# Kernel optimization log

Measured on AMD Instinct MI355X. Metric: run time of the kernel, lower is better.

## Reference

```python
import jax, jax.numpy as jnp
import numpy as np

DIM = 1024
DEPTH = 6
HEADS = 16
MLP_DIM = 4096
EPS = 1e-5


def setup_inputs() -> dict:
    key = jax.random.key(0)
    ks = jax.random.split(key, 8)
    d, L, f = DIM, DEPTH, MLP_DIM
    s = lambda fan_in: 1.0 / np.sqrt(fan_in)
    inp = {
        "x": jax.random.normal(ks[0], (4, 1024, d), dtype=jnp.float32),
        "ln1_w": jnp.ones((L, d), jnp.float32),
        "ln1_b": jnp.zeros((L, d), jnp.float32),
        "qkv_w": jax.random.normal(ks[1], (L, d, 3 * d), jnp.float32) * s(d),
        "qkv_b": jnp.zeros((L, 3 * d), jnp.float32),
        "proj_w": jax.random.normal(ks[2], (L, d, d), jnp.float32) * s(d),
        "proj_b": jnp.zeros((L, d), jnp.float32),
        "ln2_w": jnp.ones((L, d), jnp.float32),
        "ln2_b": jnp.zeros((L, d), jnp.float32),
        "mlp_w1": jax.random.normal(ks[3], (L, d, f), jnp.float32) * s(d),
        "mlp_b1": jax.random.normal(ks[4], (L, f), jnp.float32) * 1e-6,
        "mlp_w2": jax.random.normal(ks[5], (L, f, d), jnp.float32) * s(f),
        "mlp_b2": jax.random.normal(ks[6], (L, d), jnp.float32) * 1e-6,
    }
    return inp


def _layer_norm(x, w, b):
    mu = jnp.mean(x, axis=-1, keepdims=True)
    var = jnp.mean(jnp.square(x - mu), axis=-1, keepdims=True)
    return (x - mu) * jax.lax.rsqrt(var + EPS) * w + b


def _block(x, ln1_w, ln1_b, qkv_w, qkv_b, proj_w, proj_b,
           ln2_w, ln2_b, mlp_w1, mlp_b1, mlp_w2, mlp_b2):
    b, n, d = x.shape
    h = HEADS
    hd = d // h
    scale = d ** (-0.5)  # note: original scales by dim**-0.5, not head_dim**-0.5
    # attention sublayer (pre-LN + residual)
    y = _layer_norm(x, ln1_w, ln1_b)
    qkv = y @ qkv_w + qkv_b                      # [b, n, 3d]
    qkv = qkv.reshape(b, n, 3, h, hd)            # matches 'b n (qkv h d)'
    q, k, v = (jnp.moveaxis(qkv[:, :, i], 1, 2) for i in range(3))  # [b, h, n, hd]
    dots = jnp.einsum('bhid,bhjd->bhij', q, k) * scale
    attn = jax.nn.softmax(dots, axis=-1)
    out = jnp.einsum('bhij,bhjd->bhid', attn, v)
    out = jnp.moveaxis(out, 1, 2).reshape(b, n, d)
    x = x + out @ proj_w + proj_b
    # MLP sublayer (pre-LN + residual)
    y = _layer_norm(x, ln2_w, ln2_b)
    y = jax.nn.gelu(y @ mlp_w1 + mlp_b1, approximate=False)
    x = x + y @ mlp_w2 + mlp_b2
    return x


def reference(x, ln1_w, ln1_b, qkv_w, qkv_b, proj_w, proj_b,
              ln2_w, ln2_b, mlp_w1, mlp_b1, mlp_w2, mlp_b2):
    for l in range(DEPTH):
        x = _block(x, ln1_w[l], ln1_b[l], qkv_w[l], qkv_b[l],
                   proj_w[l], proj_b[l], ln2_w[l], ln2_b[l],
                   mlp_w1[l], mlp_b1[l], mlp_w2[l], mlp_b2[l])
    return x
```

## Files before the change

### kernel.cpp

```cpp
#include <hip/hip_runtime.h>

typedef __attribute__((ext_vector_type(8))) short short8;
typedef __attribute__((ext_vector_type(4))) float floatx4;

#define DIM   1024
#define SEQ   1024
#define BATCH 4
#define NHEAD 16
#define HDIM  64
#define MLPD  4096
#define DEPTH 6
#define MTOK  (BATCH*SEQ)

__device__ __forceinline__ unsigned short f2bf(float f) {
    union { float f; unsigned u; } v; v.f = f;
    unsigned r = v.u + 0x7fffu + ((v.u >> 16) & 1u);
    return (unsigned short)(r >> 16);
}

__device__ __forceinline__ void gld16(const void* g, void* l) {
    __builtin_amdgcn_global_load_lds(
        (const __attribute__((address_space(1))) unsigned int*)g,
        (__attribute__((address_space(3))) unsigned int*)l, 16, 0, 0);
}

__global__ __launch_bounds__(256) void ln_kernel(
    const float* __restrict__ x, const float* __restrict__ w,
    const float* __restrict__ b, unsigned short* __restrict__ y)
{
    __shared__ float red[8];
    const int row = blockIdx.x;
    const int t = threadIdx.x;
    const float4 v = ((const float4*)(x + (size_t)row * DIM))[t];
    float s = v.x + v.y + v.z + v.w;
#pragma unroll
    for (int m = 1; m < 64; m <<= 1) s += __shfl_xor(s, m);
    if ((t & 63) == 0) red[t >> 6] = s;
    __syncthreads();
    const float mu = (red[0] + red[1] + red[2] + red[3]) * (1.0f / DIM);
    const float d0 = v.x - mu, d1 = v.y - mu, d2 = v.z - mu, d3 = v.w - mu;
    float q = d0 * d0 + d1 * d1 + d2 * d2 + d3 * d3;
#pragma unroll
    for (int m = 1; m < 64; m <<= 1) q += __shfl_xor(q, m);
    if ((t & 63) == 0) red[4 + (t >> 6)] = q;
    __syncthreads();
    const float var = (red[4] + red[5] + red[6] + red[7]) * (1.0f / DIM);
    const float rs = rsqrtf(var + 1e-5f);
    const float4 wv = ((const float4*)w)[t];
    const float4 bv = ((const float4*)b)[t];
    ushort4 o;
    o.x = f2bf(d0 * rs * wv.x + bv.x);
    o.y = f2bf(d1 * rs * wv.y + bv.y);
    o.z = f2bf(d2 * rs * wv.z + bv.z);
    o.w = f2bf(d3 * rs * wv.w + bv.w);
    ((ushort4*)(y + (size_t)row * DIM))[t] = o;
}

__global__ __launch_bounds__(256) void wtrans_kernel(
    const float* __restrict__ W, unsigned short* __restrict__ Wt, int K, int N)
{
    __shared__ float tile[64][65];
    const int n0 = blockIdx.x * 64, k0 = blockIdx.y * 64;
    const int t = threadIdx.x;
#pragma unroll
    for (int p = t; p < 1024; p += 256) {
        const int k = p >> 4, nq = (p & 15) * 4;
        const float4 v = *(const float4*)&W[(size_t)(k0 + k) * N + n0 + nq];
        tile[k][nq + 0] = v.x; tile[k][nq + 1] = v.y;
        tile[k][nq + 2] = v.z; tile[k][nq + 3] = v.w;
    }
    __syncthreads();
#pragma unroll
    for (int p = t; p < 1024; p += 256) {
        const int n = p >> 4, kq = (p & 15) * 4;
        ushort4 o;
        o.x = f2bf(tile[kq + 0][n]); o.y = f2bf(tile[kq + 1][n]);
        o.z = f2bf(tile[kq + 2][n]); o.w = f2bf(tile[kq + 3][n]);
        *(ushort4*)&Wt[(size_t)(n0 + n) * K + k0 + kq] = o;
    }
}

template <int MODE>
__global__ __launch_bounds__(256) void gemm_pipe(
    const unsigned short* __restrict__ A, const unsigned short* __restrict__ Bt,
    const float* __restrict__ bias, void* __restrict__ Cout,
    int M, int K, int N)
{
    __shared__ __align__(16) unsigned short Al[2 * 128 * 32];
    __shared__ __align__(16) unsigned short Bl[2 * 128 * 32];

    const int bm = blockIdx.y * 128, bn = blockIdx.x * 128;
    const int tid = threadIdx.x;
    const int lane = tid & 63, wid = tid >> 6;
    const int lm = lane & 15, quad = lane >> 4;
    const int wm = (wid >> 1) * 64, wn = (wid & 1) * 64;

    floatx4 acc[4][4] = {};

    const unsigned short* gA = A + (size_t)(bm + wid * 32 + (lane >> 2)) * K + (lane & 3) * 8;
    const unsigned short* gB = Bt + (size_t)(bn + wid * 32 + (lane >> 2)) * K + (lane & 3) * 8;
    const int wof = wid * 1024;

    gld16(gA, &Al[wof]);
    gld16(gA + (size_t)16 * K, &Al[wof + 512]);
    gld16(gB, &Bl[wof]);
    gld16(gB + (size_t)16 * K, &Bl[wof + 512]);

    const int nk = K >> 5;
    for (int i = 0; i < nk; i++) {
        __syncthreads();
        const int cur = (i & 1) * 4096;
        if (i + 1 < nk) {
            const int nxt = ((i + 1) & 1) * 4096;
            const int kt = (i + 1) * 32;
            gld16(gA + kt, &Al[nxt + wof]);
            gld16(gA + (size_t)16 * K + kt, &Al[nxt + wof + 512]);
            gld16(gB + kt, &Bl[nxt + wof]);
            gld16(gB + (size_t)16 * K + kt, &Bl[nxt + wof + 512]);
        }
        short8 af[4], bf[4];
#pragma unroll
        for (int t = 0; t < 4; t++)
            af[t] = *(const short8*)&Al[cur + (wm + t * 16 + lm) * 32 + quad * 8];
#pragma unroll
        for (int t = 0; t < 4; t++)
            bf[t] = *(const short8*)&Bl[cur + (wn + t * 16 + lm) * 32 + quad * 8];
#pragma unroll
        for (int t = 0; t < 4; t++)
#pragma unroll
            for (int j = 0; j < 4; j++)
                acc[t][j] = __builtin_amdgcn_mfma_f32_16x16x32_bf16(
                    af[t], bf[j], acc[t][j], 0, 0, 0);
    }

#pragma unroll
    for (int i = 0; i < 4; i++) {
        const int row = bm + wm + i * 16 + quad * 4;
#pragma unroll
        for (int j = 0; j < 4; j++) {
            const int col = bn + wn + j * 16 + lm;
            const float bb = bias[col];
#pragma unroll
            for (int r = 0; r < 4; r++) {
                float v = acc[i][j][r] + bb;
                const size_t idx = (size_t)(row + r) * N + col;
                if constexpr (MODE == 0) {
                    ((unsigned short*)Cout)[idx] = f2bf(v);
                } else if constexpr (MODE == 1) {
                    const float g = 0.5f * v * (1.0f + erff(v * 0.70710678118654752f));
                    ((unsigned short*)Cout)[idx] = f2bf(g);
                } else {
                    ((float*)Cout)[idx] += v;
                }
            }
        }
    }
}

__global__ __launch_bounds__(256) void vtrans_kernel(
    const unsigned short* __restrict__ qkv, unsigned short* __restrict__ Vt)
{
    __shared__ unsigned short tile[64][65];
    const int bh = blockIdx.x, nt = blockIdx.y;
    const int b = bh >> 4, h = bh & 15;
    const int t = threadIdx.x;
#pragma unroll
    for (int p = t; p < 4096; p += 256) {
        const int n = p >> 6, c = p & 63;
        tile[n][c] = qkv[(size_t)(b * SEQ + nt * 64 + n) * (3 * DIM) + 2 * DIM + h * HDIM + c];
    }
    __syncthreads();
#pragma unroll
    for (int p = t; p < 4096; p += 256) {
        const int hd = p >> 6, n = p & 63;
        Vt[((size_t)bh * HDIM + hd) * SEQ + nt * 64 + n] = tile[n][hd];
    }
}

__global__ __launch_bounds__(256) void attn_kernel(
    const unsigned short* __restrict__ qkv, const unsigned short* __restrict__ Vt,
    unsigned short* __restrict__ O)
{
    __shared__ __align__(16) unsigned short P[2][4][16 * 40];
    const int bh = blockIdx.x;
    const int b = bh >> 4, h = bh & 15;
    const int tid = threadIdx.x, lane = tid & 63, wid = tid >> 6;
    const int lm = lane & 15, quad = lane >> 4;
    const int q0 = (blockIdx.y * 4 + wid) * 16;

    const unsigned short* Qbase = qkv + (size_t)(b * SEQ) * (3 * DIM) + h * HDIM;
    const unsigned short* Kbase = Qbase + DIM;
    const unsigned short* Vbase = Vt + (size_t)bh * HDIM * SEQ;

    short8 aq[2];
#pragma unroll
    for (int t = 0; t < 2; t++)
        aq[t] = *(const short8*)&Qbase[(size_t)(q0 + lm) * (3 * DIM) + t * 32 + quad * 8];

    short8 ones;
#pragma unroll
    for (int t = 0; t < 8; t++) ones[t] = (short)0x3F80;

    floatx4 o[4] = {};
    floatx4 sacc = {};
    const float scale = 0.03125f;
    const float M = 3.0f;

    short8 k0f[4], v0f[4], k1f[4], v1f[4];

    auto loadKV = [&](short8* kf, short8* vf, int kt) {
#pragma unroll
        for (int s = 0; s < 2; s++)
#pragma unroll
            for (int t = 0; t < 2; t++)
                kf[s * 2 + t] = *(const short8*)&Kbase[(size_t)(kt + s * 16 + lm) * (3 * DIM) + t * 32 + quad * 8];
#pragma unroll
        for (int ti = 0; ti < 4; ti++)
            vf[ti] = *(const short8*)&Vbase[(size_t)(ti * 16 + lm) * SEQ + kt + quad * 8];
    };

    auto compute = [&](const short8* kf, const short8* vf, unsigned short* Pw) {
        floatx4 s0 = {}, s1 = {};
        s0 = __builtin_amdgcn_mfma_f32_16x16x32_bf16(aq[0], kf[0], s0, 0, 0, 0);
        s0 = __builtin_amdgcn_mfma_f32_16x16x32_bf16(aq[1], kf[1], s0, 0, 0, 0);
        s1 = __builtin_amdgcn_mfma_f32_16x16x32_bf16(aq[0], kf[2], s1, 0, 0, 0);
        s1 = __builtin_amdgcn_mfma_f32_16x16x32_bf16(aq[1], kf[3], s1, 0, 0, 0);
#pragma unroll
        for (int r = 0; r < 4; r++) {
            Pw[(quad * 4 + r) * 40 + lm]      = f2bf(__expf(fmaf(s0[r], scale, -M)));
            Pw[(quad * 4 + r) * 40 + 16 + lm] = f2bf(__expf(fmaf(s1[r], scale, -M)));
        }
        const short8 pa = *(const short8*)&Pw[lm * 40 + quad * 8];
        sacc = __builtin_amdgcn_mfma_f32_16x16x32_bf16(pa, ones, sacc, 0, 0, 0);
#pragma unroll
        for (int ti = 0; ti < 4; ti++)
            o[ti] = __builtin_amdgcn_mfma_f32_16x16x32_bf16(pa, vf[ti], o[ti], 0, 0, 0);
    };

    loadKV(k0f, v0f, 0);
    for (int kt = 0; kt < SEQ; kt += 64) {
        loadKV(k1f, v1f, kt + 32);
        compute(k0f, v0f, P[0][wid]);
        if (kt + 64 < SEQ) loadKV(k0f, v0f, kt + 64);
        compute(k1f, v1f, P[1][wid]);
    }

#pragma unroll
    for (int r = 0; r < 4; r++) {
        const float inv = 1.0f / sacc[r];
        const int qrow = q0 + quad * 4 + r;
        const size_t orow = (size_t)(b * SEQ + qrow) * DIM + h * HDIM;
#pragma unroll
        for (int ti = 0; ti < 4; ti++)
            O[orow + ti * 16 + lm] = f2bf(o[ti][r] * inv);
    }
}

extern "C" void kernel_launch(void* const* d_in, const int* in_sizes, int n_in,
                              void* d_out, int out_size, void* d_ws, size_t ws_size,
                              hipStream_t stream)
{
    (void)in_sizes; (void)n_in; (void)out_size; (void)ws_size;
    const float* x      = (const float*)d_in[0];
    const float* ln1_w  = (const float*)d_in[1];
    const float* ln1_b  = (const float*)d_in[2];
    const float* qkv_w  = (const float*)d_in[3];
    const float* qkv_b  = (const float*)d_in[4];
    const float* proj_w = (const float*)d_in[5];
    const float* proj_b = (const float*)d_in[6];
    const float* ln2_w  = (const float*)d_in[7];
    const float* ln2_b  = (const float*)d_in[8];
    const float* mlp_w1 = (const float*)d_in[9];
    const float* mlp_b1 = (const float*)d_in[10];
    const float* mlp_w2 = (const float*)d_in[11];
    const float* mlp_b2 = (const float*)d_in[12];

    char* p = (char*)d_ws;
    float* xbuf = (float*)p;                    p += (size_t)MTOK * DIM * 4;
    unsigned short* y = (unsigned short*)p;     p += (size_t)MTOK * DIM * 2;
    unsigned short* big = (unsigned short*)p;   p += (size_t)MTOK * MLPD * 2;
    unsigned short* Vt = (unsigned short*)p;    p += (size_t)MTOK * DIM * 2;
    unsigned short* attno = (unsigned short*)p; p += (size_t)MTOK * DIM * 2;
    unsigned short* qkvT = (unsigned short*)p;  p += (size_t)DIM * 3 * DIM * 2;
    unsigned short* projT = (unsigned short*)p; p += (size_t)DIM * DIM * 2;
    unsigned short* mlp1T = (unsigned short*)p; p += (size_t)DIM * MLPD * 2;
    unsigned short* mlp2T = (unsigned short*)p; p += (size_t)MLPD * DIM * 2;

    hipMemcpyAsync(xbuf, x, (size_t)MTOK * DIM * 4, hipMemcpyDeviceToDevice, stream);

    for (int l = 0; l < DEPTH; l++) {
        wtrans_kernel<<<dim3(3 * DIM / 64, DIM / 64), 256, 0, stream>>>(
            qkv_w + (size_t)l * DIM * 3 * DIM, qkvT, DIM, 3 * DIM);
        wtrans_kernel<<<dim3(DIM / 64, DIM / 64), 256, 0, stream>>>(
            proj_w + (size_t)l * DIM * DIM, projT, DIM, DIM);
        wtrans_kernel<<<dim3(MLPD / 64, DIM / 64), 256, 0, stream>>>(
            mlp_w1 + (size_t)l * DIM * MLPD, mlp1T, DIM, MLPD);
        wtrans_kernel<<<dim3(DIM / 64, MLPD / 64), 256, 0, stream>>>(
            mlp_w2 + (size_t)l * MLPD * DIM, mlp2T, MLPD, DIM);

        ln_kernel<<<MTOK, 256, 0, stream>>>(xbuf, ln1_w + l * DIM, ln1_b + l * DIM, y);
        gemm_pipe<0><<<dim3(3 * DIM / 128, MTOK / 128), 256, 0, stream>>>(
            y, qkvT, qkv_b + (size_t)l * 3 * DIM, big, MTOK, DIM, 3 * DIM);
        vtrans_kernel<<<dim3(64, 16), 256, 0, stream>>>(big, Vt);
        attn_kernel<<<dim3(64, 16), 256, 0, stream>>>(big, Vt, attno);
        gemm_pipe<2><<<dim3(DIM / 128, MTOK / 128), 256, 0, stream>>>(
            attno, projT, proj_b + (size_t)l * DIM, xbuf, MTOK, DIM, DIM);
        ln_kernel<<<MTOK, 256, 0, stream>>>(xbuf, ln2_w + l * DIM, ln2_b + l * DIM, y);
        gemm_pipe<1><<<dim3(MLPD / 128, MTOK / 128), 256, 0, stream>>>(
            y, mlp1T, mlp_b1 + (size_t)l * MLPD, big, MTOK, DIM, MLPD);
        gemm_pipe<2><<<dim3(DIM / 128, MTOK / 128), 256, 0, stream>>>(
            big, mlp2T, mlp_b2 + (size_t)l * DIM, xbuf, MTOK, MLPD, DIM);
    }
    hipMemcpyAsync(d_out, xbuf, (size_t)MTOK * DIM * 4, hipMemcpyDeviceToDevice, stream);
}
```

Before: 2.511 ms.

## Process 32 query rows per wave with 64-key tiles in attention kernel

Each wave in the attention kernel now handles two 16-row query tiles instead of one, so every K and V fragment loaded from global memory is reused across 32 query rows. The key tile per iteration grows from 32 to 64 keys, with a larger P staging buffer in LDS. The explicit register double-buffering of K/V loads is removed in favour of a simple loop, and the grid is halved along the query dimension. The intent is to halve global K/V traffic per query. In exchange the kernel uses more registers, exposes load latency unless the compiler schedules around it, and launches half as many blocks.

```diff
diff --git a/kernel.cpp b/kernel.cpp
--- a/kernel.cpp
+++ b/kernel.cpp
@@ -181,79 +181,92 @@
     const unsigned short* __restrict__ qkv, const unsigned short* __restrict__ Vt,
     unsigned short* __restrict__ O)
 {
-    __shared__ __align__(16) unsigned short P[2][4][16 * 40];
+    __shared__ __align__(16) unsigned short P[2][4][32 * 72];
     const int bh = blockIdx.x;
     const int b = bh >> 4, h = bh & 15;
     const int tid = threadIdx.x, lane = tid & 63, wid = tid >> 6;
     const int lm = lane & 15, quad = lane >> 4;
-    const int q0 = (blockIdx.y * 4 + wid) * 16;
+    const int q0 = (blockIdx.y * 4 + wid) * 32;
 
     const unsigned short* Qbase = qkv + (size_t)(b * SEQ) * (3 * DIM) + h * HDIM;
     const unsigned short* Kbase = Qbase + DIM;
     const unsigned short* Vbase = Vt + (size_t)bh * HDIM * SEQ;
 
-    short8 aq[2];
-#pragma unroll
-    for (int t = 0; t < 2; t++)
-        aq[t] = *(const short8*)&Qbase[(size_t)(q0 + lm) * (3 * DIM) + t * 32 + quad * 8];
+    short8 aq[2][2];
+#pragma unroll
+    for (int qt = 0; qt < 2; qt++)
+#pragma unroll
+        for (int t = 0; t < 2; t++)
+            aq[qt][t] = *(const short8*)&Qbase[(size_t)(q0 + qt * 16 + lm) * (3 * DIM) + t * 32 + quad * 8];
 
     short8 ones;
 #pragma unroll
     for (int t = 0; t < 8; t++) ones[t] = (short)0x3F80;
 
-    floatx4 o[4] = {};
-    floatx4 sacc = {};
+    floatx4 o[2][4] = {};
+    floatx4 sacc[2] = {};
     const float scale = 0.03125f;
     const float M = 3.0f;
 
-    short8 k0f[4], v0f[4], k1f[4], v1f[4];
-
-    auto loadKV = [&](short8* kf, short8* vf, int kt) {
-#pragma unroll
-        for (int s = 0; s < 2; s++)
+    for (int i = 0; i < SEQ / 64; i++) {
+        const int kt = i * 64;
+        short8 bk[4][2];
+#pragma unroll
+        for (int s = 0; s < 4; s++)
 #pragma unroll
             for (int t = 0; t < 2; t++)
-                kf[s * 2 + t] = *(const short8*)&Kbase[(size_t)(kt + s * 16 + lm) * (3 * DIM) + t * 32 + quad * 8];
-#pragma unroll
-        for (int ti = 0; ti < 4; ti++)
-            vf[ti] = *(const short8*)&Vbase[(size_t)(ti * 16 + lm) * SEQ + kt + quad * 8];
-    };
-
-    auto compute = [&](const short8* kf, const short8* vf, unsigned short* Pw) {
-        floatx4 s0 = {}, s1 = {};
-        s0 = __builtin_amdgcn_mfma_f32_16x16x32_bf16(aq[0], kf[0], s0, 0, 0, 0);
-        s0 = __builtin_amdgcn_mfma_f32_16x16x32_bf16(aq[1], kf[1], s0, 0, 0, 0);
-        s1 = __builtin_amdgcn_mfma_f32_16x16x32_bf16(aq[0], kf[2], s1, 0, 0, 0);
-        s1 = __builtin_amdgcn_mfma_f32_16x16x32_bf16(aq[1], kf[3], s1, 0, 0, 0);
+                bk[s][t] = *(const short8*)&Kbase[(size_t)(kt + s * 16 + lm) * (3 * DIM) + t * 32 + quad * 8];
+        short8 bv[4][2];
+#pragma unroll
+        for (int ht = 0; ht < 4; ht++)
+#pragma unroll
+            for (int kh = 0; kh < 2; kh++)
+                bv[ht][kh] = *(const short8*)&Vbase[(size_t)(ht * 16 + lm) * SEQ + kt + kh * 32 + quad * 8];
+
+        unsigned short* Pw = P[i & 1][wid];
+#pragma unroll
+        for (int qt = 0; qt < 2; qt++)
+#pragma unroll
+            for (int s = 0; s < 4; s++) {
+                floatx4 sv = {};
+                sv = __builtin_amdgcn_mfma_f32_16x16x32_bf16(aq[qt][0], bk[s][0], sv, 0, 0, 0);
+                sv = __builtin_amdgcn_mfma_f32_16x16x32_bf16(aq[qt][1], bk[s][1], sv, 0, 0, 0);
+#pragma unroll
+                for (int r = 0; r < 4; r++)
+                    Pw[(qt * 16 + quad * 4 + r) * 72 + s * 16 + lm] =
+                        f2bf(__expf(fmaf(sv[r], scale, -M)));
+            }
+        short8 pa[2][2];
+#pragma unroll
+        for (int qt = 0; qt < 2; qt++)
+#pragma unroll
+            for (int kh = 0; kh < 2; kh++)
+                pa[qt][kh] = *(const short8*)&Pw[(qt * 16 + lm) * 72 + kh * 32 + quad * 8];
+#pragma unroll
+        for (int qt = 0; qt < 2; qt++) {
+            sacc[qt] = __builtin_amdgcn_mfma_f32_16x16x32_bf16(pa[qt][0], ones, sacc[qt], 0, 0, 0);
+            sacc[qt] = __builtin_amdgcn_mfma_f32_16x16x32_bf16(pa[qt][1], ones, sacc[qt], 0, 0, 0);
+        }
+#pragma unroll
+        for (int qt = 0; qt < 2; qt++)
+#pragma unroll
+            for (int ht = 0; ht < 4; ht++) {
+                o[qt][ht] = __builtin_amdgcn_mfma_f32_16x16x32_bf16(pa[qt][0], bv[ht][0], o[qt][ht], 0, 0, 0);
+                o[qt][ht] = __builtin_amdgcn_mfma_f32_16x16x32_bf16(pa[qt][1], bv[ht][1], o[qt][ht], 0, 0, 0);
+            }
+    }
+
+#pragma unroll
+    for (int qt = 0; qt < 2; qt++)
 #pragma unroll
         for (int r = 0; r < 4; r++) {
-            Pw[(quad * 4 + r) * 40 + lm]      = f2bf(__expf(fmaf(s0[r], scale, -M)));
-            Pw[(quad * 4 + r) * 40 + 16 + lm] = f2bf(__expf(fmaf(s1[r], scale, -M)));
+            const float inv = 1.0f / sacc[qt][r];
+            const int qrow = q0 + qt * 16 + quad * 4 + r;
+            const size_t orow = (size_t)(b * SEQ + qrow) * DIM + h * HDIM;
+#pragma unroll
+            for (int ti = 0; ti < 4; ti++)
+                O[orow + ti * 16 + lm] = f2bf(o[qt][ti][r] * inv);
         }
-        const short8 pa = *(const short8*)&Pw[lm * 40 + quad * 8];
-        sacc = __builtin_amdgcn_mfma_f32_16x16x32_bf16(pa, ones, sacc, 0, 0, 0);
-#pragma unroll
-        for (int ti = 0; ti < 4; ti++)
-            o[ti] = __builtin_amdgcn_mfma_f32_16x16x32_bf16(pa, vf[ti], o[ti], 0, 0, 0);
-    };
-
-    loadKV(k0f, v0f, 0);
-    for (int kt = 0; kt < SEQ; kt += 64) {
-        loadKV(k1f, v1f, kt + 32);
-        compute(k0f, v0f, P[0][wid]);
-        if (kt + 64 < SEQ) loadKV(k0f, v0f, kt + 64);
-        compute(k1f, v1f, P[1][wid]);
-    }
-
-#pragma unroll
-    for (int r = 0; r < 4; r++) {
-        const float inv = 1.0f / sacc[r];
-        const int qrow = q0 + quad * 4 + r;
-        const size_t orow = (size_t)(b * SEQ + qrow) * DIM + h * HDIM;
-#pragma unroll
-        for (int ti = 0; ti < 4; ti++)
-            O[orow + ti * 16 + lm] = f2bf(o[ti][r] * inv);
-    }
 }
 
 extern "C" void kernel_launch(void* const* d_in, const int* in_sizes, int n_in,
@@ -302,7 +315,7 @@
         gemm_pipe<0><<<dim3(3 * DIM / 128, MTOK / 128), 256, 0, stream>>>(
             y, qkvT, qkv_b + (size_t)l * 3 * DIM, big, MTOK, DIM, 3 * DIM);
         vtrans_kernel<<<dim3(64, 16), 256, 0, stream>>>(big, Vt);
-        attn_kernel<<<dim3(64, 16), 256, 0, stream>>>(big, Vt, attno);
+        attn_kernel<<<dim3(64, 8), 256, 0, stream>>>(big, Vt, attno);
         gemm_pipe<2><<<dim3(DIM / 128, MTOK / 128), 256, 0, stream>>>(
             attno, projT, proj_b + (size_t)l * DIM, xbuf, MTOK, DIM, DIM);
         ln_kernel<<<MTOK, 256, 0, stream>>>(xbuf, ln2_w + l * DIM, ln2_b + l * DIM, y);
```

Result: faster. 2.188 ms (-12.9%).
